# Kernel optimization log

Measured on AMD Instinct MI355X. Metric: run time of the kernel, lower is better.

Reference implementation:

```python
import jax, jax.numpy as jnp
import numpy as np

C = 36   # num_classes
H = 256  # hidden_dim


def setup_inputs() -> dict:
    key = jax.random.key(0)
    ks = jax.random.split(key, 12)
    B, L, Dl, Dg = 32, 196, 1024, 1024
    s = lambda d: 1.0 / np.sqrt(d)
    return {
        "local_features": jax.random.normal(ks[0], (B, L, Dl), jnp.float32),
        "global_average_pool": jax.random.normal(ks[1], (B, Dg), jnp.float32),
        "Wl": jax.random.normal(ks[2], (Dl, C * H), jnp.float32) * s(Dl),
        "bl": jax.random.normal(ks[3], (C * H,), jnp.float32) * s(Dl),
        "Wg": jax.random.normal(ks[4], (Dg, C * H), jnp.float32) * s(Dg),
        "bg": jax.random.normal(ks[5], (C * H,), jnp.float32) * s(Dg),
        "Wh": jax.random.normal(ks[6], (H, H), jnp.float32) * s(H),
        "bh": jax.random.normal(ks[7], (H,), jnp.float32) * s(H),
        "Wr": jax.random.normal(ks[8], (H, 4), jnp.float32) * s(H),
        "br": jax.random.normal(ks[9], (4,), jnp.float32) * s(H),
        "Wc": jax.random.normal(ks[10], (H, 1), jnp.float32) * s(H),
        "bc": jax.random.normal(ks[11], (1,), jnp.float32) * s(H),
    }


def reference(local_features, global_average_pool, Wl, bl, Wg, bg, Wh, bh, Wr, br, Wc, bc):
    B, L, _ = local_features.shape
    # global projection -> [B, C, H]
    xg = (global_average_pool @ Wg + bg).reshape(B, C, H)
    # local projection -> [B, L, C, H] -> [B, C, L, H]
    xl = (local_features @ Wl + bl).reshape(B, L, C, H).transpose(0, 2, 1, 3)
    # per-class attention scores over locations: [B, C, L]
    dot = jnp.einsum('bch,bclh->bcl', xg, xl)
    attn = jax.nn.softmax(dot, axis=-1)
    # attention-weighted sum over locations: [B, C, H]
    ws = jnp.einsum('bcl,bclh->bch', attn, xl)
    hid = jax.nn.relu(ws @ Wh + bh)
    bbox_coords = (hid @ Wr + br).reshape(B, C * 4)   # [B, 4C]
    bbox_presence = (hid @ Wc + bc)[..., 0]           # [B, C]
    return bbox_coords, bbox_presence
```

## Files before the change

kernel.cpp:

```cpp
#include <hip/hip_runtime.h>
#include <hip/hip_bf16.h>
#include <stdint.h>

#define NCLS 36
#define HDIM 256
#define BSZ  32
#define LLOC 196
#define DIN  1024
#define NCH  9216

#define XG_N 294912
#define SC_N 225792
#define V_N  1179648

__global__ __launch_bounds__(256) void kB_xg_part(
    const float* __restrict__ Wg, const float* __restrict__ gap,
    float* __restrict__ xg_part) {
  const int n  = blockIdx.x * 256 + threadIdx.x;
  const int kc = blockIdx.y * 128;
  const int b0 = blockIdx.z * 16;
  float acc[16] = {0,0,0,0,0,0,0,0,0,0,0,0,0,0,0,0};
  const float* wp = Wg + (size_t)kc * NCH + n;
  const float* gp = gap + (size_t)b0 * DIN + kc;
  for (int k4 = 0; k4 < 32; ++k4) {
    float w0 = wp[(size_t)(k4 * 4 + 0) * NCH];
    float w1 = wp[(size_t)(k4 * 4 + 1) * NCH];
    float w2 = wp[(size_t)(k4 * 4 + 2) * NCH];
    float w3 = wp[(size_t)(k4 * 4 + 3) * NCH];
    #pragma unroll
    for (int bi = 0; bi < 16; ++bi) {
      float4 g = *(const float4*)&gp[(size_t)bi * DIN + k4 * 4];
      acc[bi] += g.x * w0 + g.y * w1 + g.z * w2 + g.w * w3;
    }
  }
  #pragma unroll
  for (int bi = 0; bi < 16; ++bi)
    xg_part[(size_t)blockIdx.y * XG_N + (size_t)(b0 + bi) * NCH + n] = acc[bi];
}

__global__ void kBr_xg(const float* __restrict__ xg_part,
                       const float* __restrict__ bg, float* __restrict__ xg) {
  int i = blockIdx.x * 256 + threadIdx.x;
  float s = bg[i % NCH];
  #pragma unroll
  for (int p = 0; p < 8; ++p) s += xg_part[(size_t)p * XG_N + i];
  xg[i] = s;
}

__global__ __launch_bounds__(256) void kC_V(
    const float* __restrict__ Wl, const float* __restrict__ xg,
    float* __restrict__ V) {
  const int c  = blockIdx.x;
  const int k  = blockIdx.y * 256 + threadIdx.x;
  const int b0 = blockIdx.z * 16;
  float acc[16] = {0,0,0,0,0,0,0,0,0,0,0,0,0,0,0,0};
  const float* wl = Wl + (size_t)k * NCH + c * HDIM;
  const float* xp = xg + (size_t)b0 * NCH + c * HDIM;
  for (int j = 0; j < 64; ++j) {
    float4 w = *(const float4*)&wl[j * 4];
    #pragma unroll
    for (int bi = 0; bi < 16; ++bi) {
      float4 x = *(const float4*)&xp[(size_t)bi * NCH + j * 4];
      acc[bi] += w.x * x.x + w.y * x.y + w.z * x.z + w.w * x.w;
    }
  }
  #pragma unroll
  for (int bi = 0; bi < 16; ++bi)
    V[(size_t)((b0 + bi) * NCLS + c) * DIN + k] = acc[bi];
}

__global__ __launch_bounds__(256) void kD_scores(
    const float* __restrict__ local, const float* __restrict__ V,
    float* __restrict__ sc_part) {
  const int b  = blockIdx.x;
  const int cg = blockIdx.y;
  const int ks = blockIdx.z;
  const int l  = threadIdx.x;
  if (l >= LLOC) return;
  const float* lp = local + (size_t)(b * LLOC + l) * DIN + ks * 128;
  const float* vp = V + (size_t)(b * NCLS + cg * 12) * DIN + ks * 128;
  float acc[12] = {0,0,0,0,0,0,0,0,0,0,0,0};
  for (int j = 0; j < 32; ++j) {
    float4 a = *(const float4*)&lp[j * 4];
    #pragma unroll
    for (int ci = 0; ci < 12; ++ci) {
      float4 v = *(const float4*)&vp[(size_t)ci * DIN + j * 4];
      acc[ci] += a.x * v.x + a.y * v.y + a.z * v.z + a.w * v.w;
    }
  }
  #pragma unroll
  for (int ci = 0; ci < 12; ++ci)
    sc_part[(size_t)ks * SC_N + (size_t)(b * NCLS + cg * 12 + ci) * LLOC + l] = acc[ci];
}

__global__ __launch_bounds__(64) void kE_softmax(
    const float* __restrict__ sc_part, float* __restrict__ attn2) {
  const int b = blockIdx.x, c = blockIdx.y, t = threadIdx.x;
  const size_t base = (size_t)(b * NCLS + c) * LLOC;
  float sc[4];
  int nl = 0;
  float m = -1e30f;
  for (int l = t; l < LLOC; l += 64) {
    float s = 0.f;
    #pragma unroll
    for (int p = 0; p < 8; ++p) s += sc_part[(size_t)p * SC_N + base + l];
    sc[nl++] = s; m = fmaxf(m, s);
  }
  #pragma unroll
  for (int off = 32; off >= 1; off >>= 1) m = fmaxf(m, __shfl_xor(m, off));
  float sum = 0.f;
  for (int i = 0; i < nl; ++i) { sc[i] = __expf(sc[i] - m); sum += sc[i]; }
  #pragma unroll
  for (int off = 32; off >= 1; off >>= 1) sum += __shfl_xor(sum, off);
  float inv = 1.0f / sum;
  nl = 0;
  for (int l = t; l < LLOC; l += 64) attn2[base + l] = sc[nl++] * inv;
}

__global__ __launch_bounds__(256) void kF_U(
    const float* __restrict__ local, const float* __restrict__ attn2,
    float* __restrict__ U) {
  const int b = blockIdx.x, cg = blockIdx.z;
  const int k = blockIdx.y * 256 + threadIdx.x;
  float acc[12] = {0,0,0,0,0,0,0,0,0,0,0,0};
  const float* lp = local + (size_t)b * LLOC * DIN + k;
  const float* ap = attn2 + (size_t)(b * NCLS + cg * 12) * LLOC;
  for (int l4 = 0; l4 < 49; ++l4) {
    float a0 = lp[(size_t)(l4 * 4 + 0) * DIN];
    float a1 = lp[(size_t)(l4 * 4 + 1) * DIN];
    float a2 = lp[(size_t)(l4 * 4 + 2) * DIN];
    float a3 = lp[(size_t)(l4 * 4 + 3) * DIN];
    #pragma unroll
    for (int ci = 0; ci < 12; ++ci) {
      float4 w = *(const float4*)&ap[(size_t)ci * LLOC + l4 * 4];
      acc[ci] += a0 * w.x + a1 * w.y + a2 * w.z + a3 * w.w;
    }
  }
  #pragma unroll
  for (int ci = 0; ci < 12; ++ci)
    U[(size_t)(b * NCLS + cg * 12 + ci) * DIN + k] = acc[ci];
}

__global__ __launch_bounds__(256) void kG_ws(
    const float* __restrict__ Wl, const float* __restrict__ U,
    float* __restrict__ wsh_part) {
  const int c  = blockIdx.x;
  const int kc = blockIdx.y * 128;
  const int b0 = blockIdx.z * 16;
  const int h  = threadIdx.x;
  float acc[16] = {0,0,0,0,0,0,0,0,0,0,0,0,0,0,0,0};
  const float* wp = Wl + (size_t)kc * NCH + c * HDIM + h;
  const float* up = U + (size_t)(b0 * NCLS + c) * DIN + kc;
  for (int k4 = 0; k4 < 32; ++k4) {
    float w0 = wp[(size_t)(k4 * 4 + 0) * NCH];
    float w1 = wp[(size_t)(k4 * 4 + 1) * NCH];
    float w2 = wp[(size_t)(k4 * 4 + 2) * NCH];
    float w3 = wp[(size_t)(k4 * 4 + 3) * NCH];
    #pragma unroll
    for (int bi = 0; bi < 16; ++bi) {
      float4 u = *(const float4*)&up[(size_t)bi * NCLS * DIN + k4 * 4];
      acc[bi] += u.x * w0 + u.y * w1 + u.z * w2 + u.w * w3;
    }
  }
  #pragma unroll
  for (int bi = 0; bi < 16; ++bi)
    wsh_part[(size_t)blockIdx.y * XG_N + (size_t)(b0 + bi) * NCH + c * HDIM + h] = acc[bi];
}

__global__ __launch_bounds__(256) void kH_heads(
    const float* __restrict__ Wh, const float* __restrict__ bh,
    const float* __restrict__ Wr, const float* __restrict__ br,
    const float* __restrict__ Wc, const float* __restrict__ bc,
    const float* __restrict__ bl,
    const float* __restrict__ wsh_part, float* __restrict__ out) {
  __shared__ float ws_s[3][HDIM];
  __shared__ float hid_s[3][HDIM];
  const int b = blockIdx.x, c0 = blockIdx.y * 3;
  const int j = threadIdx.x;

  #pragma unroll
  for (int ci = 0; ci < 3; ++ci) {
    size_t base = (size_t)b * NCH + (c0 + ci) * HDIM + j;
    float s = bl[(c0 + ci) * HDIM + j];
    #pragma unroll
    for (int p = 0; p < 8; ++p) s += wsh_part[(size_t)p * XG_N + base];
    ws_s[ci][j] = s;
  }
  __syncthreads();

  float acc[3] = {0,0,0};
  for (int h = 0; h < HDIM; ++h) {
    float whj = Wh[(size_t)h * HDIM + j];
    acc[0] += ws_s[0][h] * whj;
    acc[1] += ws_s[1][h] * whj;
    acc[2] += ws_s[2][h] * whj;
  }
  float bj = bh[j];
  #pragma unroll
  for (int ci = 0; ci < 3; ++ci) hid_s[ci][j] = fmaxf(acc[ci] + bj, 0.0f);
  __syncthreads();

  const int r = j >> 6, j0 = j & 63;
  for (int ci = 0; ci < 3; ++ci) {
    const int c = c0 + ci;
    float s = 0.f;
    #pragma unroll
    for (int m = 0; m < 4; ++m)
      s += hid_s[ci][j0 + 64 * m] * Wr[(j0 + 64 * m) * 4 + r];
    #pragma unroll
    for (int off = 32; off >= 1; off >>= 1) s += __shfl_xor(s, off);
    if (j0 == 0) out[(size_t)b * (NCLS * 4) + c * 4 + r] = s + br[r];
    if (r == 0) {
      float p = 0.f;
      #pragma unroll
      for (int m = 0; m < 4; ++m)
        p += hid_s[ci][j0 + 64 * m] * Wc[j0 + 64 * m];
      #pragma unroll
      for (int off = 32; off >= 1; off >>= 1) p += __shfl_xor(p, off);
      if (j0 == 0) out[BSZ * NCLS * 4 + b * NCLS + c] = p + bc[0];
    }
  }
}

extern "C" void kernel_launch(void* const* d_in, const int* in_sizes, int n_in,
                              void* d_out, int out_size, void* d_ws, size_t ws_size,
                              hipStream_t stream) {
  const float* local = (const float*)d_in[0];
  const float* gap   = (const float*)d_in[1];
  const float* Wl    = (const float*)d_in[2];
  const float* bl    = (const float*)d_in[3];
  const float* Wg    = (const float*)d_in[4];
  const float* bg    = (const float*)d_in[5];
  const float* Wh    = (const float*)d_in[6];
  const float* bh    = (const float*)d_in[7];
  const float* Wr    = (const float*)d_in[8];
  const float* br    = (const float*)d_in[9];
  const float* Wc    = (const float*)d_in[10];
  const float* bc    = (const float*)d_in[11];
  float* out         = (float*)d_out;

  float* A  = (float*)d_ws;
  float* B  = A + (size_t)8 * XG_N;
  float* C  = B + XG_N;
  float* D  = C + V_N;
  float* E  = D + SC_N;

  kB_xg_part<<<dim3(36, 8, 2), dim3(256), 0, stream>>>(Wg, gap, A);
  kBr_xg<<<dim3(XG_N / 256), dim3(256), 0, stream>>>(A, bg, B);
  kC_V<<<dim3(36, 4, 2), dim3(256), 0, stream>>>(Wl, B, C);
  kD_scores<<<dim3(32, 3, 8), dim3(256), 0, stream>>>(local, C, A);
  kE_softmax<<<dim3(32, 36), dim3(64), 0, stream>>>(A, D);
  kF_U<<<dim3(32, 4, 3), dim3(256), 0, stream>>>(local, D, E);
  kG_ws<<<dim3(36, 8, 2), dim3(256), 0, stream>>>(Wl, E, A);
  kH_heads<<<dim3(32, 12), dim3(256), 0, stream>>>(Wh, bh, Wr, br, Wc, bc, bl, A, out);
}
```

Before: 284.7 us.

## Fuse split-K reductions into kernels and merge scores with softmax

The global projection now reduces its four K-slices through shared memory inside one kernel, which removes the separate reduction kernel and its partial buffer. The score computation and softmax are fused into one kernel with no split-K, so partial scores are never written to global memory. kC_V, kF_U and kG_ws regroup batch and class work per block, with kG_ws covering all 32 batches in one block so each Wl load feeds twice as many FMAs. In exchange the grids are smaller (for example 192 blocks for the fused score kernel, each running a 1024-long serial loop), which may leave much of the GPU idle.

Result: slower. 375.0 us (+31.7%).

```diff
diff --git a/kernel.cpp b/kernel.cpp
--- a/kernel.cpp
+++ b/kernel.cpp
@@ -10,18 +10,150 @@
 #define NCH  9216
 
 #define XG_N 294912
-#define SC_N 225792
+#define AT_N 225792
 #define V_N  1179648
 
-__global__ __launch_bounds__(256) void kB_xg_part(
+__global__ __launch_bounds__(256) void kA_xg(
     const float* __restrict__ Wg, const float* __restrict__ gap,
-    float* __restrict__ xg_part) {
-  const int n  = blockIdx.x * 256 + threadIdx.x;
+    const float* __restrict__ bg, float* __restrict__ xg) {
+  __shared__ float red[4][16][64];
+  const int tid  = threadIdx.x;
+  const int w    = __builtin_amdgcn_readfirstlane(tid >> 6);
+  const int lane = tid & 63;
+  const int n0   = blockIdx.x * 64;
+  const int b0   = blockIdx.y * 16;
+  const int k0   = w * 256;
+
+  float acc[16] = {0,0,0,0,0,0,0,0,0,0,0,0,0,0,0,0};
+  const float* wp = Wg + (size_t)k0 * NCH + n0 + lane;
+  const float* gp = gap + (size_t)b0 * DIN + k0;
+  for (int k4 = 0; k4 < 64; ++k4) {
+    float w0 = wp[(size_t)(k4 * 4 + 0) * NCH];
+    float w1 = wp[(size_t)(k4 * 4 + 1) * NCH];
+    float w2 = wp[(size_t)(k4 * 4 + 2) * NCH];
+    float w3 = wp[(size_t)(k4 * 4 + 3) * NCH];
+    #pragma unroll
+    for (int bi = 0; bi < 16; ++bi) {
+      float4 g = *(const float4*)&gp[(size_t)bi * DIN + k4 * 4];
+      acc[bi] += g.x * w0 + g.y * w1 + g.z * w2 + g.w * w3;
+    }
+  }
+  #pragma unroll
+  for (int bi = 0; bi < 16; ++bi) red[w][bi][lane] = acc[bi];
+  __syncthreads();
+  const int n = tid & 63;
+  #pragma unroll
+  for (int bb = 0; bb < 4; ++bb) {
+    int b = (tid >> 6) * 4 + bb;
+    float s = red[0][b][n] + red[1][b][n] + red[2][b][n] + red[3][b][n]
+            + bg[n0 + n];
+    xg[(size_t)(b0 + b) * NCH + n0 + n] = s;
+  }
+}
+
+__global__ __launch_bounds__(256) void kC_V(
+    const float* __restrict__ Wl, const float* __restrict__ xg,
+    float* __restrict__ V) {
+  const int c  = blockIdx.x;
+  const int k  = blockIdx.y * 128 + (threadIdx.x & 127);
+  const int b0 = __builtin_amdgcn_readfirstlane(threadIdx.x >> 7) * 16;
+  float acc[16] = {0,0,0,0,0,0,0,0,0,0,0,0,0,0,0,0};
+  const float* wl = Wl + (size_t)k * NCH + c * HDIM;
+  const float* xp = xg + (size_t)b0 * NCH + c * HDIM;
+  for (int j = 0; j < 64; ++j) {
+    float4 w = *(const float4*)&wl[j * 4];
+    #pragma unroll
+    for (int bi = 0; bi < 16; ++bi) {
+      float4 x = *(const float4*)&xp[(size_t)bi * NCH + j * 4];
+      acc[bi] += w.x * x.x + w.y * x.y + w.z * x.z + w.w * x.w;
+    }
+  }
+  #pragma unroll
+  for (int bi = 0; bi < 16; ++bi)
+    V[(size_t)((b0 + bi) * NCLS + c) * DIN + k] = acc[bi];
+}
+
+__global__ __launch_bounds__(256) void kDE_attn(
+    const float* __restrict__ local, const float* __restrict__ V,
+    float* __restrict__ attn2) {
+  __shared__ float sc_s[6][256];
+  const int b  = blockIdx.x;
+  const int c0 = blockIdx.y * 6;
+  const int l  = threadIdx.x;
+
+  if (l < LLOC) {
+    const float* lp = local + (size_t)(b * LLOC + l) * DIN;
+    const float* vp = V + (size_t)(b * NCLS + c0) * DIN;
+    float acc[6] = {0,0,0,0,0,0};
+    for (int j = 0; j < 256; ++j) {
+      float4 a = *(const float4*)&lp[j * 4];
+      #pragma unroll
+      for (int ci = 0; ci < 6; ++ci) {
+        float4 v = *(const float4*)&vp[(size_t)ci * DIN + j * 4];
+        acc[ci] += a.x * v.x + a.y * v.y + a.z * v.z + a.w * v.w;
+      }
+    }
+    #pragma unroll
+    for (int ci = 0; ci < 6; ++ci) sc_s[ci][l] = acc[ci];
+  }
+  __syncthreads();
+
+  const int w = threadIdx.x >> 6, lane = threadIdx.x & 63;
+  for (int ci = w; ci < 6; ci += 4) {
+    float m = -1e30f;
+    for (int l2 = lane; l2 < LLOC; l2 += 64) m = fmaxf(m, sc_s[ci][l2]);
+    #pragma unroll
+    for (int off = 32; off >= 1; off >>= 1) m = fmaxf(m, __shfl_xor(m, off));
+    float e[4]; int nl = 0; float sum = 0.f;
+    for (int l2 = lane; l2 < LLOC; l2 += 64) {
+      e[nl] = __expf(sc_s[ci][l2] - m); sum += e[nl]; ++nl;
+    }
+    #pragma unroll
+    for (int off = 32; off >= 1; off >>= 1) sum += __shfl_xor(sum, off);
+    float inv = 1.0f / sum;
+    nl = 0;
+    for (int l2 = lane; l2 < LLOC; l2 += 64)
+      attn2[(size_t)(b * NCLS + c0 + ci) * LLOC + l2] = e[nl++] * inv;
+  }
+}
+
+__global__ __launch_bounds__(256) void kF_U(
+    const float* __restrict__ local, const float* __restrict__ attn2,
+    float* __restrict__ U) {
+  const int b  = blockIdx.x;
+  const int k  = blockIdx.y * 128 + (threadIdx.x & 127);
+  const int c0 = __builtin_amdgcn_readfirstlane(threadIdx.x >> 7) * 18;
+  float acc[18];
+  #pragma unroll
+  for (int ci = 0; ci < 18; ++ci) acc[ci] = 0.f;
+  const float* lp = local + (size_t)b * LLOC * DIN + k;
+  const float* ap = attn2 + (size_t)(b * NCLS + c0) * LLOC;
+  for (int l4 = 0; l4 < 49; ++l4) {
+    float a0 = lp[(size_t)(l4 * 4 + 0) * DIN];
+    float a1 = lp[(size_t)(l4 * 4 + 1) * DIN];
+    float a2 = lp[(size_t)(l4 * 4 + 2) * DIN];
+    float a3 = lp[(size_t)(l4 * 4 + 3) * DIN];
+    #pragma unroll
+    for (int ci = 0; ci < 18; ++ci) {
+      float4 w = *(const float4*)&ap[(size_t)ci * LLOC + l4 * 4];
+      acc[ci] += a0 * w.x + a1 * w.y + a2 * w.z + a3 * w.w;
+    }
+  }
+  #pragma unroll
+  for (int ci = 0; ci < 18; ++ci)
+    U[(size_t)(b * NCLS + c0 + ci) * DIN + k] = acc[ci];
+}
+
+__global__ __launch_bounds__(256) void kG_ws(
+    const float* __restrict__ Wl, const float* __restrict__ U,
+    float* __restrict__ wsh_part) {
+  const int c  = blockIdx.x;
   const int kc = blockIdx.y * 128;
-  const int b0 = blockIdx.z * 16;
-  float acc[16] = {0,0,0,0,0,0,0,0,0,0,0,0,0,0,0,0};
-  const float* wp = Wg + (size_t)kc * NCH + n;
-  const float* gp = gap + (size_t)b0 * DIN + kc;
+  const int h  = threadIdx.x;
+  float acc0[16] = {0,0,0,0,0,0,0,0,0,0,0,0,0,0,0,0};
+  float acc1[16] = {0,0,0,0,0,0,0,0,0,0,0,0,0,0,0,0};
+  const float* wp = Wl + (size_t)kc * NCH + c * HDIM + h;
+  const float* up = U + (size_t)c * DIN + kc;
   for (int k4 = 0; k4 < 32; ++k4) {
     float w0 = wp[(size_t)(k4 * 4 + 0) * NCH];
     float w1 = wp[(size_t)(k4 * 4 + 1) * NCH];
@@ -29,142 +161,21 @@
     float w3 = wp[(size_t)(k4 * 4 + 3) * NCH];
     #pragma unroll
     for (int bi = 0; bi < 16; ++bi) {
-      float4 g = *(const float4*)&gp[(size_t)bi * DIN + k4 * 4];
-      acc[bi] += g.x * w0 + g.y * w1 + g.z * w2 + g.w * w3;
-    }
-  }
-  #pragma unroll
-  for (int bi = 0; bi < 16; ++bi)
-    xg_part[(size_t)blockIdx.y * XG_N + (size_t)(b0 + bi) * NCH + n] = acc[bi];
-}
-
-__global__ void kBr_xg(const float* __restrict__ xg_part,
-                       const float* __restrict__ bg, float* __restrict__ xg) {
-  int i = blockIdx.x * 256 + threadIdx.x;
-  float s = bg[i % NCH];
-  #pragma unroll
-  for (int p = 0; p < 8; ++p) s += xg_part[(size_t)p * XG_N + i];
-  xg[i] = s;
-}
-
-__global__ __launch_bounds__(256) void kC_V(
-    const float* __restrict__ Wl, const float* __restrict__ xg,
-    float* __restrict__ V) {
-  const int c  = blockIdx.x;
-  const int k  = blockIdx.y * 256 + threadIdx.x;
-  const int b0 = blockIdx.z * 16;
-  float acc[16] = {0,0,0,0,0,0,0,0,0,0,0,0,0,0,0,0};
-  const float* wl = Wl + (size_t)k * NCH + c * HDIM;
-  const float* xp = xg + (size_t)b0 * NCH + c * HDIM;
-  for (int j = 0; j < 64; ++j) {
-    float4 w = *(const float4*)&wl[j * 4];
-    #pragma unroll
-    for (int bi = 0; bi < 16; ++bi) {
-      float4 x = *(const float4*)&xp[(size_t)bi * NCH + j * 4];
-      acc[bi] += w.x * x.x + w.y * x.y + w.z * x.z + w.w * x.w;
-    }
-  }
-  #pragma unroll
-  for (int bi = 0; bi < 16; ++bi)
-    V[(size_t)((b0 + bi) * NCLS + c) * DIN + k] = acc[bi];
-}
-
-__global__ __launch_bounds__(256) void kD_scores(
-    const float* __restrict__ local, const float* __restrict__ V,
-    float* __restrict__ sc_part) {
-  const int b  = blockIdx.x;
-  const int cg = blockIdx.y;
-  const int ks = blockIdx.z;
-  const int l  = threadIdx.x;
-  if (l >= LLOC) return;
-  const float* lp = local + (size_t)(b * LLOC + l) * DIN + ks * 128;
-  const float* vp = V + (size_t)(b * NCLS + cg * 12) * DIN + ks * 128;
-  float acc[12] = {0,0,0,0,0,0,0,0,0,0,0,0};
-  for (int j = 0; j < 32; ++j) {
-    float4 a = *(const float4*)&lp[j * 4];
-    #pragma unroll
-    for (int ci = 0; ci < 12; ++ci) {
-      float4 v = *(const float4*)&vp[(size_t)ci * DIN + j * 4];
-      acc[ci] += a.x * v.x + a.y * v.y + a.z * v.z + a.w * v.w;
-    }
-  }
-  #pragma unroll
-  for (int ci = 0; ci < 12; ++ci)
-    sc_part[(size_t)ks * SC_N + (size_t)(b * NCLS + cg * 12 + ci) * LLOC + l] = acc[ci];
-}
-
-__global__ __launch_bounds__(64) void kE_softmax(
-    const float* __restrict__ sc_part, float* __restrict__ attn2) {
-  const int b = blockIdx.x, c = blockIdx.y, t = threadIdx.x;
-  const size_t base = (size_t)(b * NCLS + c) * LLOC;
-  float sc[4];
-  int nl = 0;
-  float m = -1e30f;
-  for (int l = t; l < LLOC; l += 64) {
-    float s = 0.f;
-    #pragma unroll
-    for (int p = 0; p < 8; ++p) s += sc_part[(size_t)p * SC_N + base + l];
-    sc[nl++] = s; m = fmaxf(m, s);
-  }
-  #pragma unroll
-  for (int off = 32; off >= 1; off >>= 1) m = fmaxf(m, __shfl_xor(m, off));
-  float sum = 0.f;
-  for (int i = 0; i < nl; ++i) { sc[i] = __expf(sc[i] - m); sum += sc[i]; }
-  #pragma unroll
-  for (int off = 32; off >= 1; off >>= 1) sum += __shfl_xor(sum, off);
-  float inv = 1.0f / sum;
-  nl = 0;
-  for (int l = t; l < LLOC; l += 64) attn2[base + l] = sc[nl++] * inv;
-}
-
-__global__ __launch_bounds__(256) void kF_U(
-    const float* __restrict__ local, const float* __restrict__ attn2,
-    float* __restrict__ U) {
-  const int b = blockIdx.x, cg = blockIdx.z;
-  const int k = blockIdx.y * 256 + threadIdx.x;
-  float acc[12] = {0,0,0,0,0,0,0,0,0,0,0,0};
-  const float* lp = local + (size_t)b * LLOC * DIN + k;
-  const float* ap = attn2 + (size_t)(b * NCLS + cg * 12) * LLOC;
-  for (int l4 = 0; l4 < 49; ++l4) {
-    float a0 = lp[(size_t)(l4 * 4 + 0) * DIN];
-    float a1 = lp[(size_t)(l4 * 4 + 1) * DIN];
-    float a2 = lp[(size_t)(l4 * 4 + 2) * DIN];
-    float a3 = lp[(size_t)(l4 * 4 + 3) * DIN];
-    #pragma unroll
-    for (int ci = 0; ci < 12; ++ci) {
-      float4 w = *(const float4*)&ap[(size_t)ci * LLOC + l4 * 4];
-      acc[ci] += a0 * w.x + a1 * w.y + a2 * w.z + a3 * w.w;
-    }
-  }
-  #pragma unroll
-  for (int ci = 0; ci < 12; ++ci)
-    U[(size_t)(b * NCLS + cg * 12 + ci) * DIN + k] = acc[ci];
-}
-
-__global__ __launch_bounds__(256) void kG_ws(
-    const float* __restrict__ Wl, const float* __restrict__ U,
-    float* __restrict__ wsh_part) {
-  const int c  = blockIdx.x;
-  const int kc = blockIdx.y * 128;
-  const int b0 = blockIdx.z * 16;
-  const int h  = threadIdx.x;
-  float acc[16] = {0,0,0,0,0,0,0,0,0,0,0,0,0,0,0,0};
-  const float* wp = Wl + (size_t)kc * NCH + c * HDIM + h;
-  const float* up = U + (size_t)(b0 * NCLS + c) * DIN + kc;
-  for (int k4 = 0; k4 < 32; ++k4) {
-    float w0 = wp[(size_t)(k4 * 4 + 0) * NCH];
-    float w1 = wp[(size_t)(k4 * 4 + 1) * NCH];
-    float w2 = wp[(size_t)(k4 * 4 + 2) * NCH];
-    float w3 = wp[(size_t)(k4 * 4 + 3) * NCH];
-    #pragma unroll
-    for (int bi = 0; bi < 16; ++bi) {
       float4 u = *(const float4*)&up[(size_t)bi * NCLS * DIN + k4 * 4];
-      acc[bi] += u.x * w0 + u.y * w1 + u.z * w2 + u.w * w3;
-    }
-  }
-  #pragma unroll
-  for (int bi = 0; bi < 16; ++bi)
-    wsh_part[(size_t)blockIdx.y * XG_N + (size_t)(b0 + bi) * NCH + c * HDIM + h] = acc[bi];
+      acc0[bi] += u.x * w0 + u.y * w1 + u.z * w2 + u.w * w3;
+    }
+    #pragma unroll
+    for (int bi = 0; bi < 16; ++bi) {
+      float4 u = *(const float4*)&up[(size_t)(bi + 16) * NCLS * DIN + k4 * 4];
+      acc1[bi] += u.x * w0 + u.y * w1 + u.z * w2 + u.w * w3;
+    }
+  }
+  const size_t base = (size_t)blockIdx.y * XG_N + c * HDIM + h;
+  #pragma unroll
+  for (int bi = 0; bi < 16; ++bi) {
+    wsh_part[base + (size_t)bi * NCH]        = acc0[bi];
+    wsh_part[base + (size_t)(bi + 16) * NCH] = acc1[bi];
+  }
 }
 
 __global__ __launch_bounds__(256) void kH_heads(
@@ -239,18 +250,16 @@
   const float* bc    = (const float*)d_in[11];
   float* out         = (float*)d_out;
 
-  float* A  = (float*)d_ws;
-  float* B  = A + (size_t)8 * XG_N;
-  float* C  = B + XG_N;
-  float* D  = C + V_N;
-  float* E  = D + SC_N;
-
-  kB_xg_part<<<dim3(36, 8, 2), dim3(256), 0, stream>>>(Wg, gap, A);
-  kBr_xg<<<dim3(XG_N / 256), dim3(256), 0, stream>>>(A, bg, B);
-  kC_V<<<dim3(36, 4, 2), dim3(256), 0, stream>>>(Wl, B, C);
-  kD_scores<<<dim3(32, 3, 8), dim3(256), 0, stream>>>(local, C, A);
-  kE_softmax<<<dim3(32, 36), dim3(64), 0, stream>>>(A, D);
-  kF_U<<<dim3(32, 4, 3), dim3(256), 0, stream>>>(local, D, E);
-  kG_ws<<<dim3(36, 8, 2), dim3(256), 0, stream>>>(Wl, E, A);
-  kH_heads<<<dim3(32, 12), dim3(256), 0, stream>>>(Wh, bh, Wr, br, Wc, bc, bl, A, out);
-}
+  float* xg    = (float*)d_ws;
+  float* V     = xg + XG_N;
+  float* attn2 = V + V_N;
+  float* U     = attn2 + AT_N;
+  float* wshp  = U + V_N;
+
+  kA_xg  <<<dim3(144, 2), dim3(256), 0, stream>>>(Wg, gap, bg, xg);
+  kC_V   <<<dim3(36, 8),  dim3(256), 0, stream>>>(Wl, xg, V);
+  kDE_attn<<<dim3(32, 6), dim3(256), 0, stream>>>(local, V, attn2);
+  kF_U   <<<dim3(32, 8),  dim3(256), 0, stream>>>(local, attn2, U);
+  kG_ws  <<<dim3(36, 8),  dim3(256), 0, stream>>>(Wl, U, wshp);
+  kH_heads<<<dim3(32, 12), dim3(256), 0, stream>>>(Wh, bh, Wr, br, Wc, bc, bl, wshp, out);
+}
```
